# Kernel tuning notes

Measured on AMD Instinct MI355X. Metric: run time of the kernel, lower is better.

## Reference

```python
import jax, jax.numpy as jnp
import numpy as np

LAYERS = [3, 1024, 512, 256, 128, 1]
WIDTHS = [3, 1024, 1024, 1024, 1024, 1]  # width per BsPINN: 2^(i-1)*Layers[i]
N = 131072


def _mask(num_blocks, bs1, bs2):
    # block-diagonal mask of ones, built statically (constant under jit)
    return jnp.asarray(np.kron(np.eye(num_blocks, dtype=np.float32),
                               np.ones((bs1, bs2), dtype=np.float32)))


def _xavier(key, shape, fan_in, fan_out):
    lim = np.sqrt(6.0 / (fan_in + fan_out)).astype(np.float32)
    return jax.random.uniform(key, shape, jnp.float32, -lim, lim)


def setup_inputs() -> dict:
    key = jax.random.key(0)
    ks = jax.random.split(key, 6)
    inp = {
        "X": jax.random.uniform(ks[0], (N, 3), dtype=jnp.float32),
        "lb_X": jnp.zeros((3,), jnp.float32),
        "ub_X": jnp.ones((3,), jnp.float32),
    }
    for i in range(5):
        # xavier scale per sub-block Layers[i] x Layers[i+1], as in the torch init
        inp[f"W{i}"] = _xavier(ks[i + 1], (WIDTHS[i], WIDTHS[i + 1]),
                               LAYERS[i], LAYERS[i + 1])
        inp[f"b{i}"] = jnp.zeros((1, WIDTHS[i + 1]), jnp.float32)
    return inp


def reference(X, lb_X, ub_X, W0, b0, W1, b1, W2, b2, W3, b3, W4, b4):
    # masks for hidden layers l=2,3: 2 blocks of 512x512, 4 blocks of 256x256
    m2 = _mask(2, LAYERS[2], 2 * LAYERS[3])   # [1024,1024]
    m3 = _mask(4, LAYERS[3], 2 * LAYERS[4])   # [1024,1024]
    h = 2.0 * (X - lb_X) / (ub_X - lb_X) - 1.0  # [N,3]
    h = jnp.sin(h @ W0 + b0)            # [N,1024] dense
    h = jnp.sin(h @ W1 + b1)            # [N,1024] dense
    h = jnp.sin(h @ (W2 * m2) + b2)     # [N,1024] block-diag (2 blocks)
    h = jnp.sin(h @ (W3 * m3) + b3)     # [N,1024] block-diag (4 blocks)
    return h @ W4 + b4                  # [N,1]
```

## Files before the change

### kernel.cpp

```cpp
#include <hip/hip_runtime.h>

typedef _Float16 f16x8 __attribute__((ext_vector_type(8)));
typedef _Float16 f16x4 __attribute__((ext_vector_type(4)));
typedef __fp16  fp16x2 __attribute__((ext_vector_type(2)));
typedef float f32x4 __attribute__((ext_vector_type(4)));
typedef unsigned int u32;

#define N_TOTAL 131072

__global__ __launch_bounds__(512) void pack_weights(
    const float* __restrict__ W1, const float* __restrict__ W2,
    const float* __restrict__ W3, _Float16* __restrict__ WF1,
    _Float16* __restrict__ WF2, _Float16* __restrict__ WF3) {
  int t = blockIdx.x * 512 + threadIdx.x;
  const float* src; _Float16* dst; int idx, ct, kt, lane, kbase;
  if (t < 131072) {
    idx = t; src = W1; dst = WF1;
    ct = idx >> 11; kt = (idx >> 6) & 31; lane = idx & 63; kbase = 0;
  } else if (t < 196608) {
    idx = t - 131072; src = W2; dst = WF2;
    ct = idx >> 10; kt = (idx >> 6) & 15; lane = idx & 63;
    kbase = (ct >= 32) ? 512 : 0;
  } else {
    idx = t - 196608; src = W3; dst = WF3;
    ct = idx >> 9; kt = (idx >> 6) & 7; lane = idx & 63;
    kbase = (ct >> 4) << 8;
  }
  int c  = ct * 16 + (lane & 15);
  int k0 = kbase + kt * 32 + ((lane >> 4) << 3);
  f16x8 v;
#pragma unroll
  for (int j = 0; j < 8; ++j) v[j] = (_Float16)src[(size_t)(k0 + j) * 1024 + c];
  *reinterpret_cast<f16x8*>(dst + (size_t)idx * 8) = v;
}

template <int KTFULL>
__device__ __forceinline__ void kloop(const _Float16* __restrict__ WF, char* hb,
                                      f32x4 (&acc)[4][4], int ct0, int lane,
                                      int nkt, int ktW0, u32 ldsk0) {
  const f16x8* wf = reinterpret_cast<const f16x8*>(WF) +
                    (u32)((ct0 * KTFULL + ktW0) * 64 + lane);
  const int arow = lane & 15;
  const int koff = (lane >> 4) << 3;
  const u32 abase = (u32)(arow * 1024);
  const u32 axor  = (u32)(arow << 4);

#pragma unroll 1
  for (int kt = 0; kt < nkt; ++kt) {
    f16x8 w[4];
#pragma unroll
    for (int cf = 0; cf < 4; ++cf)
      w[cf] = wf[(u32)(cf * KTFULL) * 64u + (u32)kt * 64u];
    u32 kb = ldsk0 + (u32)(kt * 64) + (u32)(koff * 2);
    f16x8 h[4];
#pragma unroll
    for (int rf = 0; rf < 4; ++rf) {
      u32 addr = ((u32)(rf * 16384) + abase + kb) ^ axor;
      h[rf] = *reinterpret_cast<const f16x8*>(hb + addr);
    }
    __builtin_amdgcn_s_setprio(1);
#pragma unroll
    for (int cf = 0; cf < 4; ++cf)
#pragma unroll
      for (int rf = 0; rf < 4; ++rf)
        acc[cf][rf] = __builtin_amdgcn_mfma_f32_16x16x32_f16(w[cf], h[rf],
                                                             acc[cf][rf], 0, 0, 0);
    __builtin_amdgcn_s_setprio(0);
  }
}

__global__
__attribute__((amdgpu_flat_work_group_size(512, 512), amdgpu_waves_per_eu(4, 4)))
void bspinn_fused(
    const float* __restrict__ X, const float* __restrict__ lb,
    const float* __restrict__ ub,
    const float* __restrict__ W0, const float* __restrict__ b0,
    const _Float16* __restrict__ WF1, const float* __restrict__ b1,
    const _Float16* __restrict__ WF2, const float* __restrict__ b2,
    const _Float16* __restrict__ WF3, const float* __restrict__ b3,
    const float* __restrict__ W4, float* __restrict__ P) {
  __shared__ alignas(16) char hb[64 * 1024];
  __shared__ float xs[64 * 4];
  __shared__ float partials[8 * 64];

  const int tid  = threadIdx.x;
  const int lane = tid & 63;
  const int wid  = tid >> 6;
  const int tile = blockIdx.x >> 1;
  const int half = blockIdx.x & 1;
  const int r0   = tile * 64;

  if (tid < 192) {
    int r = tid / 3, j = tid - r * 3;
    float x = X[(size_t)r0 * 3 + tid];
    xs[r * 4 + j] = 2.0f * (x - lb[j]) / (ub[j] - lb[j]) - 1.0f;
  }
  __syncthreads();

  auto layer1 = [&](int cbase) {
    int c0l = (tid & 255) * 2;
    int rb  = (tid >> 8) * 32;
    int cg  = cbase + c0l;
    float wa0 = W0[cg],        wb0 = W0[cg + 1];
    float wa1 = W0[1024 + cg], wb1 = W0[1025 + cg];
    float wa2 = W0[2048 + cg], wb2 = W0[2049 + cg];
    float ba = b0[cg], bbv = b0[cg + 1];
#pragma unroll 4
    for (int rr2 = 0; rr2 < 32; ++rr2) {
      int r = rb + rr2;
      float x0 = xs[r * 4], x1 = xs[r * 4 + 1], x2 = xs[r * 4 + 2];
      float va = __sinf(fmaf(x2, wa2, fmaf(x1, wa1, fmaf(x0, wa0, ba))));
      float vb = __sinf(fmaf(x2, wb2, fmaf(x1, wb1, fmaf(x0, wb0, bbv))));
      union { fp16x2 h2; u32 u; } pk;
      pk.h2 = __builtin_amdgcn_cvt_pkrtz(va, vb);
      u32 addr = ((u32)(r * 1024 + c0l * 2)) ^ ((u32)((r & 15) << 4));
      *reinterpret_cast<u32*>(hb + addr) = pk.u;
    }
  };

  const int csub = (lane >> 4) << 2;
  const int rr   = lane & 15;
  const int ct0  = half * 32 + wid * 4;
  f32x4 acc[4][4];

  auto zacc = [&]() {
#pragma unroll
    for (int cf = 0; cf < 4; ++cf)
#pragma unroll
      for (int rf = 0; rf < 4; ++rf) acc[cf][rf] = f32x4{0.f, 0.f, 0.f, 0.f};
  };
  auto epi_store = [&](const float* bias) {
#pragma unroll
    for (int cf = 0; cf < 4; ++cf) {
      int c0l = wid * 64 + cf * 16 + csub;
      int cg  = half * 512 + c0l;
      f32x4 bb = *reinterpret_cast<const f32x4*>(bias + cg);
#pragma unroll
      for (int rf = 0; rf < 4; ++rf) {
        int r = rf * 16 + rr;
        float s0 = __sinf(acc[cf][rf][0] + bb[0]);
        float s1 = __sinf(acc[cf][rf][1] + bb[1]);
        float s2 = __sinf(acc[cf][rf][2] + bb[2]);
        float s3 = __sinf(acc[cf][rf][3] + bb[3]);
        union { fp16x2 h2[2]; f16x4 v; } pk;
        pk.h2[0] = __builtin_amdgcn_cvt_pkrtz(s0, s1);
        pk.h2[1] = __builtin_amdgcn_cvt_pkrtz(s2, s3);
        u32 addr = ((u32)(r * 1024 + c0l * 2)) ^ ((u32)(rr << 4));
        *reinterpret_cast<f16x4*>(hb + addr) = pk.v;
      }
    }
  };

  layer1(0);
  __syncthreads();
  zacc();
  kloop<32>(WF1, hb, acc, ct0, lane, 16, 0, 0);
  __syncthreads();
  layer1(512);
  __syncthreads();
  kloop<32>(WF1, hb, acc, ct0, lane, 16, 16, 0);
  __syncthreads();
  epi_store(b1);
  __syncthreads();

  zacc();
  kloop<16>(WF2, hb, acc, ct0, lane, 16, 0, 0);
  __syncthreads();
  epi_store(b2);
  __syncthreads();

  zacc();
  kloop<8>(WF3, hb, acc, ct0, lane, 8, 0, (u32)((wid >> 2) * 512));
  __syncthreads();
  epi_store(b3);
  __syncthreads();

  {
    int r = lane;
    u32 rb = (u32)(r * 1024);
    u32 xr = (u32)((r & 15) << 4);
    float s = 0.f;
#pragma unroll
    for (int kk = 0; kk < 64; kk += 8) {
      int kl = wid * 64 + kk;
      const float* w4p = W4 + half * 512 + kl;
      f16x8 v = *reinterpret_cast<const f16x8*>(hb + ((rb + (u32)(kl * 2)) ^ xr));
#pragma unroll
      for (int j = 0; j < 8; ++j) s = fmaf((float)v[j], w4p[j], s);
    }
    partials[wid * 64 + r] = s;
  }
  __syncthreads();
  if (tid < 64) {
    float s = 0.f;
#pragma unroll
    for (int g = 0; g < 8; ++g) s += partials[g * 64 + tid];
    P[(size_t)half * N_TOTAL + r0 + tid] = s;
  }
}

__global__ __launch_bounds__(256) void reduce_out(
    const float* __restrict__ P, const float* __restrict__ b4,
    float* __restrict__ out) {
  int i = blockIdx.x * 256 + threadIdx.x;
  out[i] = P[i] + P[N_TOTAL + i] + b4[0];
}

extern "C" void kernel_launch(void* const* d_in, const int* in_sizes, int n_in,
                              void* d_out, int out_size, void* d_ws, size_t ws_size,
                              hipStream_t stream) {
  const float* X  = (const float*)d_in[0];
  const float* lb = (const float*)d_in[1];
  const float* ub = (const float*)d_in[2];
  const float* W0 = (const float*)d_in[3];
  const float* b0 = (const float*)d_in[4];
  const float* W1 = (const float*)d_in[5];
  const float* b1 = (const float*)d_in[6];
  const float* W2 = (const float*)d_in[7];
  const float* b2 = (const float*)d_in[8];
  const float* W3 = (const float*)d_in[9];
  const float* b3 = (const float*)d_in[10];
  const float* W4 = (const float*)d_in[11];
  const float* b4 = (const float*)d_in[12];
  float* out = (float*)d_out;

  _Float16* WF1 = (_Float16*)d_ws;
  _Float16* WF2 = (_Float16*)((char*)d_ws + 2097152);
  _Float16* WF3 = (_Float16*)((char*)d_ws + 3145728);
  float*    P   = (float*)((char*)d_ws + 3670016);

  hipLaunchKernelGGL(pack_weights, dim3(448), dim3(512), 0, stream,
                     W1, W2, W3, WF1, WF2, WF3);
  hipLaunchKernelGGL(bspinn_fused, dim3((N_TOTAL / 64) * 2), dim3(512), 0, stream,
                     X, lb, ub, W0, b0, WF1, b1, WF2, b2, WF3, b3, W4, P);
  hipLaunchKernelGGL(reduce_out, dim3(N_TOTAL / 256), dim3(256), 0, stream,
                     P, b4, out);
}
```

Baseline: 482.6 us.

## Replace XOR-swizzled LDS activation layout with padded rows and fully unroll k-loops

After: 1.673 ms. 247% more time.

```diff
diff --git a/kernel.cpp b/kernel.cpp
--- a/kernel.cpp
+++ b/kernel.cpp
@@ -7,6 +7,7 @@
 typedef unsigned int u32;
 
 #define N_TOTAL 131072
+#define RSTRIDE 1040
 
 __global__ __launch_bounds__(512) void pack_weights(
     const float* __restrict__ W1, const float* __restrict__ W2,
@@ -34,30 +35,26 @@
   *reinterpret_cast<f16x8*>(dst + (size_t)idx * 8) = v;
 }
 
-template <int KTFULL>
+template <int KTFULL, int NKT>
 __device__ __forceinline__ void kloop(const _Float16* __restrict__ WF, char* hb,
                                       f32x4 (&acc)[4][4], int ct0, int lane,
-                                      int nkt, int ktW0, u32 ldsk0) {
+                                      int ktW0, u32 ldsk0) {
   const f16x8* wf = reinterpret_cast<const f16x8*>(WF) +
                     (u32)((ct0 * KTFULL + ktW0) * 64 + lane);
-  const int arow = lane & 15;
-  const int koff = (lane >> 4) << 3;
-  const u32 abase = (u32)(arow * 1024);
-  const u32 axor  = (u32)(arow << 4);
-
-#pragma unroll 1
-  for (int kt = 0; kt < nkt; ++kt) {
+  const u32 hbase = (u32)((lane & 15) * RSTRIDE) +
+                    (u32)(((lane >> 4) << 3) * 2) + ldsk0;
+
+#pragma unroll
+  for (int kt = 0; kt < NKT; ++kt) {
     f16x8 w[4];
 #pragma unroll
     for (int cf = 0; cf < 4; ++cf)
-      w[cf] = wf[(u32)(cf * KTFULL) * 64u + (u32)kt * 64u];
-    u32 kb = ldsk0 + (u32)(kt * 64) + (u32)(koff * 2);
+      w[cf] = wf[(u32)(cf * KTFULL) * 64u + (u32)(kt * 64)];
     f16x8 h[4];
 #pragma unroll
-    for (int rf = 0; rf < 4; ++rf) {
-      u32 addr = ((u32)(rf * 16384) + abase + kb) ^ axor;
-      h[rf] = *reinterpret_cast<const f16x8*>(hb + addr);
-    }
+    for (int rf = 0; rf < 4; ++rf)
+      h[rf] = *reinterpret_cast<const f16x8*>(
+          hb + hbase + (u32)(rf * 16 * RSTRIDE + kt * 64));
     __builtin_amdgcn_s_setprio(1);
 #pragma unroll
     for (int cf = 0; cf < 4; ++cf)
@@ -79,7 +76,7 @@
     const _Float16* __restrict__ WF2, const float* __restrict__ b2,
     const _Float16* __restrict__ WF3, const float* __restrict__ b3,
     const float* __restrict__ W4, float* __restrict__ P) {
-  __shared__ alignas(16) char hb[64 * 1024];
+  __shared__ alignas(16) char hb[64 * RSTRIDE];
   __shared__ float xs[64 * 4];
   __shared__ float partials[8 * 64];
 
@@ -100,11 +97,11 @@
   auto layer1 = [&](int cbase) {
     int c0l = (tid & 255) * 2;
     int rb  = (tid >> 8) * 32;
-    int cg  = cbase + c0l;
-    float wa0 = W0[cg],        wb0 = W0[cg + 1];
-    float wa1 = W0[1024 + cg], wb1 = W0[1025 + cg];
-    float wa2 = W0[2048 + cg], wb2 = W0[2049 + cg];
-    float ba = b0[cg], bbv = b0[cg + 1];
+    int cg2 = cbase + c0l;
+    float wa0 = W0[cg2],        wb0 = W0[cg2 + 1];
+    float wa1 = W0[1024 + cg2], wb1 = W0[1025 + cg2];
+    float wa2 = W0[2048 + cg2], wb2 = W0[2049 + cg2];
+    float ba = b0[cg2], bbv = b0[cg2 + 1];
 #pragma unroll 4
     for (int rr2 = 0; rr2 < 32; ++rr2) {
       int r = rb + rr2;
@@ -113,8 +110,7 @@
       float vb = __sinf(fmaf(x2, wb2, fmaf(x1, wb1, fmaf(x0, wb0, bbv))));
       union { fp16x2 h2; u32 u; } pk;
       pk.h2 = __builtin_amdgcn_cvt_pkrtz(va, vb);
-      u32 addr = ((u32)(r * 1024 + c0l * 2)) ^ ((u32)((r & 15) << 4));
-      *reinterpret_cast<u32*>(hb + addr) = pk.u;
+      *reinterpret_cast<u32*>(hb + (u32)(r * RSTRIDE + c0l * 2)) = pk.u;
     }
   };
 
@@ -133,8 +129,8 @@
 #pragma unroll
     for (int cf = 0; cf < 4; ++cf) {
       int c0l = wid * 64 + cf * 16 + csub;
-      int cg  = half * 512 + c0l;
-      f32x4 bb = *reinterpret_cast<const f32x4*>(bias + cg);
+      int cgc = half * 512 + c0l;
+      f32x4 bb = *reinterpret_cast<const f32x4*>(bias + cgc);
 #pragma unroll
       for (int rf = 0; rf < 4; ++rf) {
         int r = rf * 16 + rr;
@@ -145,8 +141,7 @@
         union { fp16x2 h2[2]; f16x4 v; } pk;
         pk.h2[0] = __builtin_amdgcn_cvt_pkrtz(s0, s1);
         pk.h2[1] = __builtin_amdgcn_cvt_pkrtz(s2, s3);
-        u32 addr = ((u32)(r * 1024 + c0l * 2)) ^ ((u32)(rr << 4));
-        *reinterpret_cast<f16x4*>(hb + addr) = pk.v;
+        *reinterpret_cast<f16x4*>(hb + (u32)(r * RSTRIDE + c0l * 2)) = pk.v;
       }
     }
   };
@@ -154,37 +149,35 @@
   layer1(0);
   __syncthreads();
   zacc();
-  kloop<32>(WF1, hb, acc, ct0, lane, 16, 0, 0);
+  kloop<32, 16>(WF1, hb, acc, ct0, lane, 0, 0);
   __syncthreads();
   layer1(512);
   __syncthreads();
-  kloop<32>(WF1, hb, acc, ct0, lane, 16, 16, 0);
+  kloop<32, 16>(WF1, hb, acc, ct0, lane, 16, 0);
   __syncthreads();
   epi_store(b1);
   __syncthreads();
 
   zacc();
-  kloop<16>(WF2, hb, acc, ct0, lane, 16, 0, 0);
+  kloop<16, 16>(WF2, hb, acc, ct0, lane, 0, 0);
   __syncthreads();
   epi_store(b2);
   __syncthreads();
 
   zacc();
-  kloop<8>(WF3, hb, acc, ct0, lane, 8, 0, (u32)((wid >> 2) * 512));
+  kloop<8, 8>(WF3, hb, acc, ct0, lane, 0, (u32)((wid >> 2) * 512));
   __syncthreads();
   epi_store(b3);
   __syncthreads();
 
   {
     int r = lane;
-    u32 rb = (u32)(r * 1024);
-    u32 xr = (u32)((r & 15) << 4);
     float s = 0.f;
 #pragma unroll
     for (int kk = 0; kk < 64; kk += 8) {
       int kl = wid * 64 + kk;
       const float* w4p = W4 + half * 512 + kl;
-      f16x8 v = *reinterpret_cast<const f16x8*>(hb + ((rb + (u32)(kl * 2)) ^ xr));
+      f16x8 v = *reinterpret_cast<const f16x8*>(hb + (u32)(r * RSTRIDE + kl * 2));
 #pragma unroll
       for (int j = 0; j < 8; ++j) s = fmaf((float)v[j], w4p[j], s);
     }
```
